# Kernel tuning notes

Measured on AMD Instinct MI355X. Metric: run time of the kernel, lower is better.

## Reference

```python
import jax, jax.numpy as jnp
import numpy as np

NPOINT = 1024
BRANCHES = [(0.4, 32), (0.8, 64)]  # (radius, nsample)
SPECS = [[67, 64, 64, 128], [67, 64, 128, 256]]  # mlp specs after use_xyz (+3)
EPS = 1e-5


def setup_inputs() -> dict:
    key = jax.random.key(0)
    ks = jax.random.split(key, 16)
    B, N, C = 8, 8192, 64
    inp = {
        "xyz": jax.random.normal(ks[0], (B, N, 3), jnp.float32),
        "features": jax.random.normal(ks[1], (B, C, N), jnp.float32),
    }
    ki = 2
    for bi, spec in enumerate(SPECS):
        for li in range(3):
            o, i = spec[li + 1], spec[li]
            inp[f"w{bi}_{li}"] = jax.random.normal(ks[ki], (o, i), jnp.float32) * (1.0 / np.sqrt(i)); ki += 1
            inp[f"g{bi}_{li}"] = jnp.ones((o,), jnp.float32)
            inp[f"b{bi}_{li}"] = jnp.zeros((o,), jnp.float32)
    return inp


def fps(pts, npoint):
    # pts: [B, N+1, 3] (mean point prepended); sequential farthest point sampling
    B, N1, _ = pts.shape

    def step(carry, _):
        dist, far = carry
        idx3 = jnp.broadcast_to(far[:, None, None], (B, 1, 3))
        centroid = jnp.take_along_axis(pts, idx3, axis=1)  # [B,1,3]
        d = jnp.sum((pts - centroid) ** 2, axis=-1)        # [B,N+1]
        dist = jnp.minimum(dist, d)
        far2 = jnp.argmax(dist, axis=-1)
        return (dist, far2), centroid[:, 0, :]

    dist0 = jnp.full((B, N1), 1e10, jnp.float32)
    far0 = jnp.zeros((B,), jnp.int32)
    _, locs = jax.lax.scan(step, (dist0, far0), None, length=npoint)
    return jnp.transpose(locs, (1, 0, 2))  # [B, npoint, 3]


def ball_query(xyz, new_xyz, radius, nsample):
    # first <=nsample indices with dist^2 < radius^2, padded with first valid (0 if none)
    B, N, _ = xyz.shape
    d2 = jnp.sum((new_xyz[:, :, None, :] - xyz[:, None, :, :]) ** 2, axis=-1)  # [B,S,N]
    score = jnp.where(d2 < radius * radius, jnp.arange(N, dtype=jnp.int32), N)
    vals, _ = jax.lax.top_k(-score, nsample)  # smallest scores = earliest valid indices
    idx = -vals                               # [B,S,nsample], N marks invalid
    first = idx[..., :1]
    first = jnp.where(first < N, first, 0)
    return jnp.where(idx < N, idx, first)


def _forward(xyz, features, params):
    mean = jnp.mean(xyz, axis=1, keepdims=True)
    pts = jnp.concatenate([mean, xyz], axis=1)          # prepend mean point
    new_xyz = jax.lax.stop_gradient(fps(pts, NPOINT))   # [B,npoint,3] (torch no_grad)
    outs = []
    for (radius, nsample), layers in zip(BRANCHES, params):
        idx = ball_query(xyz, new_xyz, radius, nsample)           # [B,S,K]
        gxyz = jax.vmap(lambda p, i: p[i])(xyz, idx)              # [B,S,K,3]
        rel = jnp.transpose(gxyz - new_xyz[:, :, None, :], (0, 3, 1, 2))  # [B,3,S,K]
        gfeat = jax.vmap(lambda f, i: f[:, i])(features, idx)     # [B,C,S,K]
        x = jnp.concatenate([rel, gfeat], axis=1)                 # [B,3+C,S,K]
        for W, g, b in layers:  # Conv2d 1x1 (no bias) + BatchNorm (train stats) + ReLU
            x = jnp.einsum('oi,bisk->bosk', W, x)
            m = jnp.mean(x, axis=(0, 2, 3), keepdims=True)
            v = jnp.var(x, axis=(0, 2, 3), keepdims=True)
            x = (x - m) / jnp.sqrt(v + EPS) * g[None, :, None, None] + b[None, :, None, None]
            x = jax.nn.relu(x)
        outs.append(jnp.max(x, axis=3))                           # [B,Cout,S]
    return new_xyz, jnp.concatenate(outs, axis=1)


def reference(xyz, features,
              w0_0, g0_0, b0_0, w0_1, g0_1, b0_1, w0_2, g0_2, b0_2,
              w1_0, g1_0, b1_0, w1_1, g1_1, b1_1, w1_2, g1_2, b1_2):
    params = [
        [(w0_0, g0_0, b0_0), (w0_1, g0_1, b0_1), (w0_2, g0_2, b0_2)],
        [(w1_0, g1_0, b1_0), (w1_1, g1_1, b1_1), (w1_2, g1_2, b1_2)],
    ]
    return _forward(xyz, features, params)
```

## Files before the change

### kernel.cpp

```cpp
#include <hip/hip_runtime.h>
#include <hip/hip_bf16.h>
#include <cstdint>


typedef __attribute__((ext_vector_type(8))) short short8;
typedef __attribute__((ext_vector_type(4))) float f32x4;
typedef __attribute__((ext_vector_type(2))) float f32x2;

__device__ __forceinline__ float bf2f(unsigned short u) {
    return __uint_as_float(((unsigned)u) << 16);
}
__device__ __forceinline__ unsigned short f2bf(float f) {
    unsigned u = __float_as_uint(f);
    return (unsigned short)((u + 0x7fffu + ((u >> 16) & 1u)) >> 16);
}

__device__ __forceinline__ float wave_red_max_f32(float v) {
#define DPPSTEP(ctrl)                                                                  \
    {                                                                                  \
        int _t = __builtin_amdgcn_update_dpp((int)0xFF800000, __float_as_int(v), ctrl, \
                                             0xf, 0xf, false);                         \
        v = fmaxf(v, __int_as_float(_t));                                              \
    }
    DPPSTEP(0x111) DPPSTEP(0x112) DPPSTEP(0x114) DPPSTEP(0x118) DPPSTEP(0x142) DPPSTEP(0x143)
#undef DPPSTEP
    return v;
}
__device__ __forceinline__ unsigned wave_red_min_u32(unsigned v) {
#define DPPSTEP(ctrl)                                                                   \
    {                                                                                   \
        unsigned _t = (unsigned)__builtin_amdgcn_update_dpp((int)0xFFFFFFFF, (int)v,    \
                                                            ctrl, 0xf, 0xf, false);     \
        v = v < _t ? v : _t;                                                            \
    }
    DPPSTEP(0x111) DPPSTEP(0x112) DPPSTEP(0x114) DPPSTEP(0x118) DPPSTEP(0x142) DPPSTEP(0x143)
#undef DPPSTEP
    return v;
}
__device__ __forceinline__ unsigned long long u64max(unsigned long long a, unsigned long long b) {
    return a > b ? a : b;
}
__device__ __forceinline__ unsigned u32min(unsigned a, unsigned b) { return a < b ? a : b; }

static const size_t OFF_WBF   = 0;
static const size_t OFF_STATS = 262144;
static const size_t STATS_BYTES = 720896;
static const size_t OFF_AFF   = 1048576;
static const size_t OFF_IDX0  = 2097152;
static const size_t OFF_IDX1  = 3145728;
static const size_t OFF_MX    = 5242880;
static const size_t OFF_MN    = 13631488;
static const size_t OFF_Y0    = 22020096;
static const size_t OFF_Y1    = 90177536;
static const size_t OFF_FEATT = 211812352;

__global__ __launch_bounds__(512) void fused_pre(
    const float* __restrict__ xyz, const float* __restrict__ feat,
    float* __restrict__ newxyz, unsigned short* __restrict__ ft,
    const float* __restrict__ w0, const float* __restrict__ w1, const float* __restrict__ w2,
    const float* __restrict__ w3, const float* __restrict__ w4, const float* __restrict__ w5,
    unsigned short* __restrict__ wb) {
    __shared__ union alignas(16) SM {
        struct {
            float ptsx[8200], ptsy[8200], ptsz[8200];
            float ldsM[16][3];
            float meanv[3];
            unsigned long long sKey[2][8];
        } f;
        float tile[64][65];
    } sm;
    const int tid = threadIdx.x;

    if (blockIdx.x >= 1032) {
        int id = (int)(blockIdx.x - 1032) * 512 + tid;
        const int psz[6] = {6144, 4096, 8192, 6144, 8192, 32768};
        const int Kp[6] = {96, 64, 64, 96, 64, 128};
        const int Ks[6] = {67, 64, 64, 67, 64, 128};
        const float* wp[6] = {w0, w1, w2, w3, w4, w5};
        int off = 0;
        for (int l = 0; l < 6; ++l) {
            if (id < off + psz[l]) {
                int e = id - off;
                int m = e / Kp[l], k = e - m * Kp[l];
                float v = (k < Ks[l]) ? wp[l][m * Ks[l] + k] : 0.f;
                wb[id] = f2bf(v);
                return;
            }
            off += psz[l];
        }
        return;
    }

    if (blockIdx.x >= 8) {
        int tb = (int)blockIdx.x - 8;
        int b = tb >> 7;
        int j0 = (tb & 127) * 64;
#pragma unroll
        for (int i = 0; i < 8; ++i) {
            int e = i * 512 + tid;
            int c = e >> 6, j = e & 63;
            sm.tile[j][c] = feat[((size_t)b * 64 + c) * 8192 + j0 + j];
        }
        __syncthreads();
#pragma unroll
        for (int i = 0; i < 8; ++i) {
            int e = i * 512 + tid;
            int j = e >> 6, c = e & 63;
            ft[((size_t)(b * 8192 + j0 + j)) * 96 + 3 + c] = f2bf(sm.tile[j][c]);
        }
        if (tid < 64) {
            int j = tid;
            size_t base = ((size_t)(b * 8192 + j0 + j)) * 96;
            const float* xp = xyz + ((size_t)b * 8192 + j0 + j) * 3;
            ft[base + 0] = f2bf(xp[0]);
            ft[base + 1] = f2bf(xp[1]);
            ft[base + 2] = f2bf(xp[2]);
        } else if (tid < 128) {
            int j = tid - 64;
            size_t base = ((size_t)(b * 8192 + j0 + j)) * 96;
            for (int c = 67; c < 96; ++c) ft[base + c] = 0;
        }
        return;
    }

    const int b = blockIdx.x;
    const int t = tid;
    const int lane = t & 63, wv = t >> 6;
    const float* xb = xyz + (size_t)b * 8192 * 3;

    f32x2 px[8], py[8], pz[8], d[8];
#pragma unroll
    for (int k = 0; k < 8; ++k) {
        int q0 = t + 512 * (2 * k);
        int q1 = t + 512 * (2 * k + 1);
        px[k].x = xb[q0 * 3 + 0]; px[k].y = xb[q1 * 3 + 0];
        py[k].x = xb[q0 * 3 + 1]; py[k].y = xb[q1 * 3 + 1];
        pz[k].x = xb[q0 * 3 + 2]; pz[k].y = xb[q1 * 3 + 2];
        d[k].x = 1e10f; d[k].y = 1e10f;
        sm.f.ptsx[q0 + 1] = px[k].x; sm.f.ptsx[q1 + 1] = px[k].y;
        sm.f.ptsy[q0 + 1] = py[k].x; sm.f.ptsy[q1 + 1] = py[k].y;
        sm.f.ptsz[q0 + 1] = pz[k].x; sm.f.ptsz[q1 + 1] = pz[k].y;
    }
    float sxA = 0.f, syA = 0.f, szA = 0.f;
    float sxB = 0.f, syB = 0.f, szB = 0.f;
    int uA = (t + 1023) & 1023;
    int uB = (t + 511) & 1023;
#pragma unroll
    for (int j = 0; j < 8; ++j) {
        int ia = uA + 1024 * j;
        int ib = uB + 1024 * j;
        sxA += xb[ia * 3 + 0]; syA += xb[ia * 3 + 1]; szA += xb[ia * 3 + 2];
        sxB += xb[ib * 3 + 0]; syB += xb[ib * 3 + 1]; szB += xb[ib * 3 + 2];
    }
#pragma unroll
    for (int off = 32; off; off >>= 1) {
        sxA += __shfl_xor(sxA, off, 64);
        syA += __shfl_xor(syA, off, 64);
        szA += __shfl_xor(szA, off, 64);
        sxB += __shfl_xor(sxB, off, 64);
        syB += __shfl_xor(syB, off, 64);
        szB += __shfl_xor(szB, off, 64);
    }
    if (lane == 0) {
        sm.f.ldsM[wv][0] = sxA; sm.f.ldsM[wv][1] = syA; sm.f.ldsM[wv][2] = szA;
        sm.f.ldsM[wv + 8][0] = sxB; sm.f.ldsM[wv + 8][1] = syB; sm.f.ldsM[wv + 8][2] = szB;
    }
    __syncthreads();
    if (t < 3) {
        float s = 0.f;
        for (int w = 0; w < 16; ++w) s += sm.f.ldsM[w][t];
        sm.f.meanv[t] = s * (1.f / 8192.f);
    }
    __syncthreads();
    float cx = sm.f.meanv[0], cy = sm.f.meanv[1], cz = sm.f.meanv[2];
    const float mmx = cx, mmy = cy, mmz = cz;
    float dm = 1e10f;
    if (t == 0) { sm.f.ptsx[0] = cx; sm.f.ptsy[0] = cy; sm.f.ptsz[0] = cz; }
    __syncthreads();

    for (int it = 0; it < 1024; ++it) {
        if (t == 0) {
            float* o = newxyz + ((size_t)b * 1024 + it) * 3;
            o[0] = cx; o[1] = cy; o[2] = cz;
        }
        f32x2 c0, c1, c2, vm2;
        c0.x = cx; c0.y = cx; c1.x = cy; c1.y = cy; c2.x = cz; c2.y = cz;
        vm2.x = -1e30f; vm2.y = -1e30f;
        {
#pragma clang fp contract(off)
#pragma unroll
            for (int k = 0; k < 8; ++k) {
                f32x2 dx = px[k] - c0;
                f32x2 dy = py[k] - c1;
                f32x2 dz = pz[k] - c2;
                f32x2 dd = (dx * dx + dy * dy) + dz * dz;
                f32x2 nd = __builtin_elementwise_min(d[k], dd);
                d[k] = nd;
                vm2 = __builtin_elementwise_max(vm2, nd);
            }
        }
        float vmax = fmaxf(vm2.x, vm2.y);
        if (t == 0) {
            float dx = __fsub_rn(mmx, cx);
            float dy = __fsub_rn(mmy, cy);
            float dz = __fsub_rn(mmz, cz);
            float dd = __fadd_rn(__fadd_rn(__fmul_rn(dx, dx), __fmul_rn(dy, dy)), __fmul_rn(dz, dz));
            dm = fminf(dm, dd);
            vmax = fmaxf(vmax, dm);
        }
        float wm = wave_red_max_f32(vmax);
        float bmaxw = __int_as_float(__builtin_amdgcn_readlane(__float_as_int(wm), 63));
        unsigned m2[8];
#pragma unroll
        for (int k = 0; k < 8; ++k) {
            unsigned i0 = (d[k].x == bmaxw) ? (unsigned)(t + 512 * (2 * k) + 1) : 0xFFFFFFFFu;
            unsigned i1 = (d[k].y == bmaxw) ? (unsigned)(t + 512 * (2 * k + 1) + 1) : 0xFFFFFFFFu;
            m2[k] = u32min(i0, i1);
        }
        unsigned n0 = u32min(m2[0], m2[1]), n1 = u32min(m2[2], m2[3]);
        unsigned n2 = u32min(m2[4], m2[5]), n3 = u32min(m2[6], m2[7]);
        unsigned mi = u32min(u32min(n0, n1), u32min(n2, n3));
        if (t == 0 && dm == bmaxw) mi = 0u;
        unsigned wmin = wave_red_min_u32(mi);
        unsigned miw = (unsigned)__builtin_amdgcn_readlane((int)wmin, 63);
        int par = it & 1;
        if (lane == 0)
            sm.f.sKey[par][wv] = ((unsigned long long)__float_as_uint(bmaxw) << 32) |
                                 (unsigned long long)(8192u - miw);
        __syncthreads();
        unsigned long long ka[8];
#pragma unroll
        for (int i = 0; i < 8; ++i) ka[i] = sm.f.sKey[par][i];
        unsigned long long p0 = u64max(ka[0], ka[1]), p1 = u64max(ka[2], ka[3]);
        unsigned long long p2 = u64max(ka[4], ka[5]), p3 = u64max(ka[6], ka[7]);
        unsigned long long kk = u64max(u64max(p0, p1), u64max(p2, p3));
        int far = 8192 - (int)(unsigned)(kk & 0xffffffffull);
        cx = sm.f.ptsx[far];
        cy = sm.f.ptsy[far];
        cz = sm.f.ptsz[far];
    }
}

__global__ void ball_query_kernel(const float* __restrict__ xyz, const float* __restrict__ newxyz,
                                  int* __restrict__ idxout, float r2, int K) {
    int wid = (blockIdx.x * blockDim.x + threadIdx.x) >> 6;
    int lane = threadIdx.x & 63;
    int b = wid >> 10;
    const float* q = newxyz + (size_t)wid * 3;
    float qx = q[0], qy = q[1], qz = q[2];
    const float* xb = xyz + (size_t)b * 8192 * 3;
    int* out = idxout + (size_t)wid * K;
    int count = 0;
    int first = 0;
    for (int base = 0; base < 8192 && count < K; base += 64) {
        int j = base + lane;
        float dx = __fsub_rn(xb[j * 3 + 0], qx);
        float dy = __fsub_rn(xb[j * 3 + 1], qy);
        float dz = __fsub_rn(xb[j * 3 + 2], qz);
        float d2 = __fadd_rn(__fadd_rn(__fmul_rn(dx, dx), __fmul_rn(dy, dy)), __fmul_rn(dz, dz));
        bool in = d2 < r2;
        unsigned long long m = __ballot(in);
        if (count == 0 && m) first = base + __ffsll((long long)m) - 1;
        if (in) {
            int pos = count + __popcll(m & ((1ull << lane) - 1ull));
            if (pos < K) out[pos] = j;
        }
        count += __popcll(m);
    }
    if (count < K) {
        int fillv = (count > 0) ? first : 0;
        for (int p = count + lane; p < K; p += 64) out[p] = fillv;
    }
}

template <int Mp, int Kp, int IN_MODE, int OUT_MODE, int KSH>
__global__ __launch_bounds__(256) void gemm_mfma(
    const unsigned short* __restrict__ Wb, const unsigned short* __restrict__ Xin,
    const float* __restrict__ aff, const int* __restrict__ idx,
    const unsigned short* __restrict__ ftp, const float* __restrict__ newxyz,
    unsigned short* __restrict__ Yout, float* __restrict__ MX, float* __restrict__ MN,
    float* __restrict__ statS, float* __restrict__ statQ) {
    constexpr int MT = Mp / 64;
    constexpr int KS = Kp / 32;
    const int tid = threadIdx.x;
    const int w = tid >> 6;
    const int lane = tid & 63;
    const int n = lane & 15;
    const int quad = lane >> 4;
    const int rbase = w * (Mp / 4);
    const long col0 = (long)blockIdx.x * 64;

    short8 a[MT][KS];
#pragma unroll
    for (int mt = 0; mt < MT; ++mt)
#pragma unroll
        for (int ks = 0; ks < KS; ++ks)
            a[mt][ks] = *(const short8*)(Wb + (size_t)(rbase + mt * 16 + n) * Kp + ks * 32 + quad * 8);

    f32x4 acc[MT][4];
#pragma unroll
    for (int mt = 0; mt < MT; ++mt)
#pragma unroll
        for (int nt = 0; nt < 4; ++nt)
#pragma unroll
            for (int r = 0; r < 4; ++r) acc[mt][nt][r] = 0.f;

    long fbase[4];
    float qv0[4], qv1[4], qv2[4];
    if constexpr (IN_MODE == 0) {
        int bb = (int)(col0 >> (KSH + 10));
#pragma unroll
        for (int nt = 0; nt < 4; ++nt) {
            long col = col0 + nt * 16 + n;
            int j = idx[col];
            fbase[nt] = ((long)bb * 8192 + j) * 96;
            long sk = col >> KSH;
            qv0[nt] = newxyz[sk * 3 + 0];
            qv1[nt] = newxyz[sk * 3 + 1];
            qv2[nt] = newxyz[sk * 3 + 2];
        }
    }

#pragma unroll
    for (int ks = 0; ks < KS; ++ks) {
        float sc[8], sh[8];
        if constexpr (IN_MODE == 1) {
#pragma unroll
            for (int e = 0; e < 8; ++e) {
                sc[e] = aff[ks * 32 + quad * 8 + e];
                sh[e] = aff[Kp + ks * 32 + quad * 8 + e];
            }
        }
#pragma unroll
        for (int nt = 0; nt < 4; ++nt) {
            short8 bfr;
            if constexpr (IN_MODE == 0) {
                bfr = *(const short8*)(ftp + fbase[nt] + ks * 32 + quad * 8);
                if (ks == 0 && quad == 0) {
                    bfr[0] = (short)f2bf(bf2f((unsigned short)bfr[0]) - qv0[nt]);
                    bfr[1] = (short)f2bf(bf2f((unsigned short)bfr[1]) - qv1[nt]);
                    bfr[2] = (short)f2bf(bf2f((unsigned short)bfr[2]) - qv2[nt]);
                }
            } else {
                long col = col0 + nt * 16 + n;
                short8 raw = *(const short8*)(Xin + col * Kp + ks * 32 + quad * 8);
#pragma unroll
                for (int e = 0; e < 8; ++e) {
                    float xf = bf2f((unsigned short)raw[e]);
                    xf = fmaxf(fmaf(xf, sc[e], sh[e]), 0.f);
                    bfr[e] = (short)f2bf(xf);
                }
            }
#pragma unroll
            for (int mt = 0; mt < MT; ++mt)
                acc[mt][nt] = __builtin_amdgcn_mfma_f32_16x16x32_bf16(a[mt][ks], bfr, acc[mt][nt], 0, 0, 0);
        }
    }

    const int slot = (int)(blockIdx.x & 127);
#pragma unroll
    for (int mt = 0; mt < MT; ++mt)
#pragma unroll
        for (int r = 0; r < 4; ++r) {
            float s = 0.f, q = 0.f;
#pragma unroll
            for (int nt = 0; nt < 4; ++nt) {
                float v = acc[mt][nt][r];
                s += v;
                q = fmaf(v, v, q);
            }
#pragma unroll
            for (int off = 1; off < 16; off <<= 1) {
                s += __shfl_xor(s, off, 16);
                q += __shfl_xor(q, off, 16);
            }
            if (n == 0) {
                int ch = rbase + mt * 16 + quad * 4 + r;
                atomicAdd(statS + (size_t)ch * 128 + slot, s);
                atomicAdd(statQ + (size_t)ch * 128 + slot, q);
            }
        }

    if constexpr (OUT_MODE == 0) {
#pragma unroll
        for (int mt = 0; mt < MT; ++mt)
#pragma unroll
            for (int nt = 0; nt < 4; ++nt) {
                long col = col0 + nt * 16 + n;
                unsigned p0 = f2bf(acc[mt][nt][0]) | ((unsigned)f2bf(acc[mt][nt][1]) << 16);
                unsigned p1 = f2bf(acc[mt][nt][2]) | ((unsigned)f2bf(acc[mt][nt][3]) << 16);
                uint2 st; st.x = p0; st.y = p1;
                *(uint2*)(Yout + col * Mp + rbase + mt * 16 + quad * 4) = st;
            }
    } else {
#pragma unroll
        for (int mt = 0; mt < MT; ++mt)
#pragma unroll
            for (int r = 0; r < 4; ++r) {
                if constexpr (KSH == 6) {
                    float mx = acc[mt][0][r], mn = acc[mt][0][r];
#pragma unroll
                    for (int nt = 1; nt < 4; ++nt) {
                        mx = fmaxf(mx, acc[mt][nt][r]);
                        mn = fminf(mn, acc[mt][nt][r]);
                    }
#pragma unroll
                    for (int off = 1; off < 16; off <<= 1) {
                        mx = fmaxf(mx, __shfl_xor(mx, off, 16));
                        mn = fminf(mn, __shfl_xor(mn, off, 16));
                    }
                    if (n == 0) {
                        int ch = rbase + mt * 16 + quad * 4 + r;
                        long g = col0 >> 6;
                        MX[(long)ch * 8192 + g] = mx;
                        MN[(long)ch * 8192 + g] = mn;
                    }
                } else {
#pragma unroll
                    for (int gh = 0; gh < 2; ++gh) {
                        float mx = fmaxf(acc[mt][2 * gh][r], acc[mt][2 * gh + 1][r]);
                        float mn = fminf(acc[mt][2 * gh][r], acc[mt][2 * gh + 1][r]);
#pragma unroll
                        for (int off = 1; off < 16; off <<= 1) {
                            mx = fmaxf(mx, __shfl_xor(mx, off, 16));
                            mn = fminf(mn, __shfl_xor(mn, off, 16));
                        }
                        if (n == 0) {
                            int ch = rbase + mt * 16 + quad * 4 + r;
                            long g = (col0 >> 5) + gh;
                            MX[(long)ch * 8192 + g] = mx;
                            MN[(long)ch * 8192 + g] = mn;
                        }
                    }
                }
            }
    }
}

__global__ void finalize_kernel(const float* __restrict__ sS, const float* __restrict__ sQ,
                                const float* __restrict__ g, const float* __restrict__ b,
                                float* __restrict__ aff, int C, float invCount) {
    int c = threadIdx.x + blockIdx.x * blockDim.x;
    if (c >= C) return;
    float s = 0.f, q = 0.f;
    for (int k = 0; k < 128; ++k) { s += sS[c * 128 + k]; q += sQ[c * 128 + k]; }
    float mean = s * invCount;
    float var = fmaxf(q * invCount - mean * mean, 0.f);
    float sc = g[c] / sqrtf(var + 1e-5f);
    float sh = b[c] - mean * sc;
    aff[c] = sc;
    aff[C + c] = sh;
}

__global__ void final_out_kernel(const float* __restrict__ MX, const float* __restrict__ MN,
                                 const float* __restrict__ aff, float* __restrict__ out1,
                                 int Cout, int cOff) {
    long i = (long)blockIdx.x * 256 + threadIdx.x;
    int c = (int)(i >> 13);
    int gidx = (int)(i & 8191);
    int b = gidx >> 10, s = gidx & 1023;
    float sc = aff[c], sh = aff[Cout + c];
    float v = fmaxf(fmaxf(sc * MX[i] + sh, sc * MN[i] + sh), 0.f);
    out1[((long)b * 384 + cOff + c) * 1024 + s] = v;
}

extern "C" void kernel_launch(void* const* d_in, const int* in_sizes, int n_in,
                              void* d_out, int out_size, void* d_ws, size_t ws_size,
                              hipStream_t stream) {
    const float* xyz = (const float*)d_in[0];
    const float* feat = (const float*)d_in[1];
    const float *W[6], *G[6], *Bi[6];
    for (int l = 0; l < 6; ++l) {
        W[l] = (const float*)d_in[2 + l * 3];
        G[l] = (const float*)d_in[3 + l * 3];
        Bi[l] = (const float*)d_in[4 + l * 3];
    }
    char* ws = (char*)d_ws;
    float* out0 = (float*)d_out;
    float* out1 = (float*)d_out + 24576;

    unsigned short* wb = (unsigned short*)(ws + OFF_WBF);
    float* stats = (float*)(ws + OFF_STATS);
    float* affine = (float*)(ws + OFF_AFF);
    int* idx0 = (int*)(ws + OFF_IDX0);
    int* idx1 = (int*)(ws + OFF_IDX1);
    float* mx = (float*)(ws + OFF_MX);
    float* mn = (float*)(ws + OFF_MN);
    unsigned short* y0 = (unsigned short*)(ws + OFF_Y0);
    unsigned short* y1 = (unsigned short*)(ws + OFF_Y1);
    unsigned short* ftp = (unsigned short*)(ws + OFF_FEATT);

    hipMemsetAsync(stats, 0, STATS_BYTES, stream);
    fused_pre<<<1160, 512, 0, stream>>>(xyz, feat, out0, ftp, W[0], W[1], W[2], W[3], W[4],
                                        W[5], wb);

    const int wOff[6] = {0, 6144, 10240, 18432, 24576, 32768};
    int stOff[6], afOff[6];
    {
        const int Cs[6] = {64, 64, 128, 64, 128, 256};
        int so = 0, ao = 0;
        for (int l = 0; l < 6; ++l) {
            stOff[l] = so; so += Cs[l] * 256;
            afOff[l] = ao; ao += Cs[l] * 2;
        }
    }

    for (int br = 0; br < 2; ++br) {
        const int K = br ? 64 : 32;
        const float radius = br ? 0.8f : 0.4f;
        const long NCOL = 8L * 1024 * K;
        int* idx = br ? idx1 : idx0;
        const int l0 = br * 3, l1 = br * 3 + 1, l2 = br * 3 + 2;
        const int M2 = br ? 256 : 128;
        const float invCount = 1.f / (float)NCOL;
        const int nblk = (int)(NCOL / 64);

        ball_query_kernel<<<2048, 256, 0, stream>>>(xyz, out0, idx, radius * radius, K);

        if (br == 0) {
            gemm_mfma<64, 96, 0, 0, 5><<<nblk, 256, 0, stream>>>(
                wb + wOff[l0], nullptr, nullptr, idx, ftp, out0, y0, nullptr, nullptr,
                stats + stOff[l0], stats + stOff[l0] + 64 * 128);
            finalize_kernel<<<1, 256, 0, stream>>>(stats + stOff[l0], stats + stOff[l0] + 64 * 128,
                                                   G[l0], Bi[l0], affine + afOff[l0], 64, invCount);
            gemm_mfma<64, 64, 1, 0, 5><<<nblk, 256, 0, stream>>>(
                wb + wOff[l1], y0, affine + afOff[l0], nullptr, nullptr, nullptr, y1, nullptr,
                nullptr, stats + stOff[l1], stats + stOff[l1] + 64 * 128);
            finalize_kernel<<<1, 256, 0, stream>>>(stats + stOff[l1], stats + stOff[l1] + 64 * 128,
                                                   G[l1], Bi[l1], affine + afOff[l1], 64, invCount);
            gemm_mfma<128, 64, 1, 1, 5><<<nblk, 256, 0, stream>>>(
                wb + wOff[l2], y1, affine + afOff[l1], nullptr, nullptr, nullptr, nullptr, mx, mn,
                stats + stOff[l2], stats + stOff[l2] + 128 * 128);
            finalize_kernel<<<1, 256, 0, stream>>>(stats + stOff[l2], stats + stOff[l2] + 128 * 128,
                                                   G[l2], Bi[l2], affine + afOff[l2], 128, invCount);
        } else {
            gemm_mfma<64, 96, 0, 0, 6><<<nblk, 256, 0, stream>>>(
                wb + wOff[l0], nullptr, nullptr, idx, ftp, out0, y0, nullptr, nullptr,
                stats + stOff[l0], stats + stOff[l0] + 64 * 128);
            finalize_kernel<<<1, 256, 0, stream>>>(stats + stOff[l0], stats + stOff[l0] + 64 * 128,
                                                   G[l0], Bi[l0], affine + afOff[l0], 64, invCount);
            gemm_mfma<128, 64, 1, 0, 6><<<nblk, 256, 0, stream>>>(
                wb + wOff[l1], y0, affine + afOff[l0], nullptr, nullptr, nullptr, y1, nullptr,
                nullptr, stats + stOff[l1], stats + stOff[l1] + 128 * 128);
            finalize_kernel<<<1, 256, 0, stream>>>(stats + stOff[l1], stats + stOff[l1] + 128 * 128,
                                                   G[l1], Bi[l1], affine + afOff[l1], 128, invCount);
            gemm_mfma<256, 128, 1, 1, 6><<<nblk, 256, 0, stream>>>(
                wb + wOff[l2], y1, affine + afOff[l1], nullptr, nullptr, nullptr, nullptr, mx, mn,
                stats + stOff[l2], stats + stOff[l2] + 256 * 128);
            finalize_kernel<<<1, 256, 0, stream>>>(stats + stOff[l2], stats + stOff[l2] + 256 * 128,
                                                   G[l2], Bi[l2], affine + afOff[l2], 256, invCount);
        }

        final_out_kernel<<<(M2 * 8192) / 256, 256, 0, stream>>>(mx, mn, affine + afOff[l2], out1,
                                                                M2, br ? 128 : 0);
    }
}
```

Baseline: 1.773 ms.

## Stage GEMM input tile in LDS once per block and buffer FPS centroids

The GEMM kernel now loads each 64-column B tile, with the gather, xyz-relative subtraction or BN-affine+ReLU, cooperatively into padded shared memory once per block. All four waves then read it from LDS instead of each wave re-gathering and re-transforming the same columns from global memory. Index, query-center and affine values are also staged in LDS. Separately, FPS writes centroids to an LDS buffer inside the loop and flushes them coalesced at the end, which removes per-iteration global stores. This costs extra LDS, which can limit occupancy, and adds block barriers.

```diff
diff --git a/kernel.cpp b/kernel.cpp
--- a/kernel.cpp
+++ b/kernel.cpp
@@ -66,6 +66,7 @@
             float ldsM[16][3];
             float meanv[3];
             unsigned long long sKey[2][8];
+            float cbuf[3072];
         } f;
         float tile[64][65];
     } sm;
@@ -180,8 +181,9 @@
 
     for (int it = 0; it < 1024; ++it) {
         if (t == 0) {
-            float* o = newxyz + ((size_t)b * 1024 + it) * 3;
-            o[0] = cx; o[1] = cy; o[2] = cz;
+            sm.f.cbuf[it * 3 + 0] = cx;
+            sm.f.cbuf[it * 3 + 1] = cy;
+            sm.f.cbuf[it * 3 + 2] = cz;
         }
         f32x2 c0, c1, c2, vm2;
         c0.x = cx; c0.y = cx; c1.x = cy; c1.y = cy; c2.x = cz; c2.y = cz;
@@ -239,6 +241,10 @@
         cy = sm.f.ptsy[far];
         cz = sm.f.ptsz[far];
     }
+    __syncthreads();
+    float* ob = newxyz + (size_t)b * 3072;
+#pragma unroll
+    for (int i = 0; i < 6; ++i) ob[t + 512 * i] = sm.f.cbuf[t + 512 * i];
 }
 
 __global__ void ball_query_kernel(const float* __restrict__ xyz, const float* __restrict__ newxyz,
@@ -282,6 +288,13 @@
     float* __restrict__ statS, float* __restrict__ statQ) {
     constexpr int MT = Mp / 64;
     constexpr int KS = Kp / 32;
+    constexpr int Kpad = Kp + 8;
+    constexpr int KC = Kp / 8;
+    constexpr int CPT = (64 * KC) / 256;
+    __shared__ unsigned short Bs[64 * Kpad];
+    __shared__ float sAux[256];
+    int* sAuxI = (int*)sAux;
+
     const int tid = threadIdx.x;
     const int w = tid >> 6;
     const int lane = tid & 63;
@@ -297,6 +310,55 @@
         for (int ks = 0; ks < KS; ++ks)
             a[mt][ks] = *(const short8*)(Wb + (size_t)(rbase + mt * 16 + n) * Kp + ks * 32 + quad * 8);
 
+    if constexpr (IN_MODE == 0) {
+        if (tid < 64) {
+            long colg = col0 + tid;
+            sAuxI[tid] = idx[colg];
+            long sk = colg >> KSH;
+            sAux[64 + tid] = newxyz[sk * 3 + 0];
+            sAux[128 + tid] = newxyz[sk * 3 + 1];
+            sAux[192 + tid] = newxyz[sk * 3 + 2];
+        }
+    } else {
+        if (tid < 2 * Kp) sAux[tid] = aff[tid];
+    }
+    __syncthreads();
+
+    if constexpr (IN_MODE == 0) {
+        const int bb = (int)(col0 >> (KSH + 10));
+#pragma unroll
+        for (int i = 0; i < CPT; ++i) {
+            int c = i * 256 + tid;
+            int col = c / KC;
+            int kc = c - col * KC;
+            int j = sAuxI[col];
+            short8 v = *(const short8*)(ftp + ((long)(bb * 8192 + j)) * 96 + kc * 8);
+            if (kc == 0) {
+                v[0] = (short)f2bf(bf2f((unsigned short)v[0]) - sAux[64 + col]);
+                v[1] = (short)f2bf(bf2f((unsigned short)v[1]) - sAux[128 + col]);
+                v[2] = (short)f2bf(bf2f((unsigned short)v[2]) - sAux[192 + col]);
+            }
+            *(short8*)(&Bs[col * Kpad + kc * 8]) = v;
+        }
+    } else {
+#pragma unroll
+        for (int i = 0; i < CPT; ++i) {
+            int c = i * 256 + tid;
+            int col = c / KC;
+            int kc = c - col * KC;
+            short8 raw = *(const short8*)(Xin + (col0 + col) * (long)Kp + kc * 8);
+            short8 v;
+#pragma unroll
+            for (int e = 0; e < 8; ++e) {
+                float xf = bf2f((unsigned short)raw[e]);
+                xf = fmaxf(fmaf(xf, sAux[kc * 8 + e], sAux[Kp + kc * 8 + e]), 0.f);
+                v[e] = (short)f2bf(xf);
+            }
+            *(short8*)(&Bs[col * Kpad + kc * 8]) = v;
+        }
+    }
+    __syncthreads();
+
     f32x4 acc[MT][4];
 #pragma unroll
     for (int mt = 0; mt < MT; ++mt)
@@ -305,52 +367,11 @@
 #pragma unroll
             for (int r = 0; r < 4; ++r) acc[mt][nt][r] = 0.f;
 
-    long fbase[4];
-    float qv0[4], qv1[4], qv2[4];
-    if constexpr (IN_MODE == 0) {
-        int bb = (int)(col0 >> (KSH + 10));
+#pragma unroll
+    for (int ks = 0; ks < KS; ++ks) {
 #pragma unroll
         for (int nt = 0; nt < 4; ++nt) {
-            long col = col0 + nt * 16 + n;
-            int j = idx[col];
-            fbase[nt] = ((long)bb * 8192 + j) * 96;
-            long sk = col >> KSH;
-            qv0[nt] = newxyz[sk * 3 + 0];
-            qv1[nt] = newxyz[sk * 3 + 1];
-            qv2[nt] = newxyz[sk * 3 + 2];
-        }
-    }
-
-#pragma unroll
-    for (int ks = 0; ks < KS; ++ks) {
-        float sc[8], sh[8];
-        if constexpr (IN_MODE == 1) {
-#pragma unroll
-            for (int e = 0; e < 8; ++e) {
-                sc[e] = aff[ks * 32 + quad * 8 + e];
-                sh[e] = aff[Kp + ks * 32 + quad * 8 + e];
-            }
-        }
-#pragma unroll
-        for (int nt = 0; nt < 4; ++nt) {
-            short8 bfr;
-            if constexpr (IN_MODE == 0) {
-                bfr = *(const short8*)(ftp + fbase[nt] + ks * 32 + quad * 8);
-                if (ks == 0 && quad == 0) {
-                    bfr[0] = (short)f2bf(bf2f((unsigned short)bfr[0]) - qv0[nt]);
-                    bfr[1] = (short)f2bf(bf2f((unsigned short)bfr[1]) - qv1[nt]);
-                    bfr[2] = (short)f2bf(bf2f((unsigned short)bfr[2]) - qv2[nt]);
-                }
-            } else {
-                long col = col0 + nt * 16 + n;
-                short8 raw = *(const short8*)(Xin + col * Kp + ks * 32 + quad * 8);
-#pragma unroll
-                for (int e = 0; e < 8; ++e) {
-                    float xf = bf2f((unsigned short)raw[e]);
-                    xf = fmaxf(fmaf(xf, sc[e], sh[e]), 0.f);
-                    bfr[e] = (short)f2bf(xf);
-                }
-            }
+            short8 bfr = *(const short8*)(&Bs[(nt * 16 + n) * Kpad + ks * 32 + quad * 8]);
 #pragma unroll
             for (int mt = 0; mt < MT; ++mt)
                 acc[mt][nt] = __builtin_amdgcn_mfma_f32_16x16x32_bf16(a[mt][ks], bfr, acc[mt][nt], 0, 0, 0);
```

After: 1.783 ms. Within noise of the previous version (+0.6%).
